# Kernel optimization log

Measured on AMD Instinct MI355X. Metric: run time of the kernel, lower is better.

## Reference

```python
import jax, jax.numpy as jnp
import numpy as np

B, N, D = 4, 4096, 1024
HEADS, DIM_HEAD = 16, 64
INNER = HEADS * DIM_HEAD
LN_EPS = 1e-5


def next_fast_len(n):
    # smallest 5-smooth integer >= n (matches scipy.fftpack.next_fast_len)
    while True:
        m = n
        for p in (2, 3, 5):
            while m % p == 0:
                m //= p
        if m == 1:
            return n
        n += 1


def setup_inputs() -> dict:
    key = jax.random.key(0)
    k = jax.random.split(key, 6)
    x = jax.random.normal(k[0], (B, N, D), dtype=jnp.float32)
    gamma = jnp.ones((D,), dtype=jnp.float32)
    beta = jnp.zeros((D,), dtype=jnp.float32)
    alpha = jax.random.normal(k[1], (HEADS,), dtype=jnp.float32)
    w_in = jax.random.normal(k[2], (INNER, D), dtype=jnp.float32) * 0.02
    w_out = jax.random.normal(k[3], (D, INNER), dtype=jnp.float32) * 0.02
    return {"x": x, "gamma": gamma, "beta": beta, "alpha": alpha, "w_in": w_in, "w_out": w_out}


def reference(x, gamma, beta, alpha, w_in, w_out):
    b, n, d = x.shape
    h, dh = HEADS, DIM_HEAD
    # LayerNorm (biased variance, eps=1e-5)
    mu = jnp.mean(x, axis=-1, keepdims=True)
    var = jnp.var(x, axis=-1, keepdims=True)
    xn = (x - mu) * jax.lax.rsqrt(var + LN_EPS) * gamma + beta
    # project_in (no bias), split heads: b n (h d) -> b h n d
    xi = jnp.einsum('bnd,ed->bne', xn, w_in)
    xi = xi.reshape(b, n, h, dh).transpose(0, 2, 1, 3)  # [b,h,n,dh]
    # exponential decay weights per head: alpha * (1-alpha)**flip(arange(n)) -> [h, n]
    a = jax.nn.sigmoid(alpha)[:, None]
    weights = a * (1.0 - a) ** jnp.arange(n - 1, -1, -1, dtype=x.dtype)[None, :]
    # FFT-based causal correlation (conv1d_fft)
    fast_len = next_fast_len(n + n - 1)
    f_x = jnp.fft.rfft(xi, n=fast_len, axis=-2)           # [b,h,L',dh] complex
    f_w = jnp.fft.rfft(weights, n=fast_len, axis=-1)      # [h,L'] complex
    out = jnp.fft.irfft(f_x * jnp.conj(f_w)[None, :, :, None], fast_len, axis=-2)
    out = jnp.roll(out, -1, axis=-2)
    out = out[:, :, fast_len - n:, :]                      # last n positions -> [b,h,n,dh]
    # merge heads and project out
    out = out.transpose(0, 2, 1, 3).reshape(b, n, h * dh)
    return jnp.einsum('bne,de->bnd', out, w_out)
```

## Files before the change

kernel.cpp:

```cpp
#include <hip/hip_runtime.h>
#include <hip/hip_bf16.h>

#define B_ 4
#define N_ 4096
#define D_ 1024
#define H_ 16
#define INNER_ 1024
#define M_ (B_ * N_)
#define CH_ 128
#define CL_ 32

using bf16x8 = __attribute__((ext_vector_type(8))) __bf16;
using f32x4  = __attribute__((ext_vector_type(4))) float;

__device__ __forceinline__ float bf2f(unsigned short v) {
  return __uint_as_float(((unsigned)v) << 16);
}
__device__ __forceinline__ unsigned short f2bf(float f) {
  __hip_bfloat16 h = __float2bfloat16(f);
  return *reinterpret_cast<unsigned short*>(&h);
}
__device__ __forceinline__ float sigm(float x) { return 1.f / (1.f + expf(-x)); }

__device__ __forceinline__ void gload_lds16(const void* g, void* l) {
  __builtin_amdgcn_global_load_lds(
      (const __attribute__((address_space(1))) unsigned int*)g,
      (__attribute__((address_space(3))) unsigned int*)l, 16, 0, 0);
}

#define W4_ ((INNER_ * D_) / 4)
__global__ __launch_bounds__(256) void cast2_kernel(
    const float* __restrict__ wa, const float* __restrict__ wb,
    __hip_bfloat16* __restrict__ oa, __hip_bfloat16* __restrict__ ob) {
  int i = blockIdx.x * 256 + threadIdx.x;
  const float* src = (i < W4_) ? wa : wb;
  __hip_bfloat16* dst = (i < W4_) ? oa : ob;
  int j = (i < W4_) ? i : i - W4_;
  float4 v = reinterpret_cast<const float4*>(src)[j];
  ushort4 o;
  o.x = f2bf(v.x); o.y = f2bf(v.y); o.z = f2bf(v.z); o.w = f2bf(v.w);
  reinterpret_cast<ushort4*>(dst)[j] = o;
}

__global__ __launch_bounds__(256) void ln_kernel(
    const float* __restrict__ x, const float* __restrict__ gamma,
    const float* __restrict__ beta, __hip_bfloat16* __restrict__ xn) {
  const long row = blockIdx.x;
  const int t = threadIdx.x;
  const float4 v = reinterpret_cast<const float4*>(x + row * D_)[t];
  float s = v.x + v.y + v.z + v.w;
  float s2 = v.x * v.x + v.y * v.y + v.z * v.z + v.w * v.w;
#pragma unroll
  for (int o = 32; o > 0; o >>= 1) {
    s += __shfl_down(s, o);
    s2 += __shfl_down(s2, o);
  }
  __shared__ float red[8];
  const int lane = t & 63, wv = t >> 6;
  if (lane == 0) { red[wv] = s; red[4 + wv] = s2; }
  __syncthreads();
  const float sum = red[0] + red[1] + red[2] + red[3];
  const float sum2 = red[4] + red[5] + red[6] + red[7];
  const float mu = sum * (1.f / D_);
  const float var = sum2 * (1.f / D_) - mu * mu;
  const float rs = rsqrtf(var + 1e-5f);
  const float4 g = reinterpret_cast<const float4*>(gamma)[t];
  const float4 bb = reinterpret_cast<const float4*>(beta)[t];
  ushort4 o;
  o.x = f2bf((v.x - mu) * rs * g.x + bb.x);
  o.y = f2bf((v.y - mu) * rs * g.y + bb.y);
  o.z = f2bf((v.z - mu) * rs * g.z + bb.z);
  o.w = f2bf((v.w - mu) * rs * g.w + bb.w);
  reinterpret_cast<ushort4*>(xn + row * D_)[t] = o;
}

__device__ __forceinline__ void stc(float* p, float v) { *p = v; }
__device__ __forceinline__ void stc(__hip_bfloat16* p, float v) { *p = __float2bfloat16(v); }

template <typename TOUT, int NT>
__global__ __launch_bounds__(512, 2) void gemm256_kernel(
    const __hip_bfloat16* __restrict__ A, const __hip_bfloat16* __restrict__ Bt,
    TOUT* __restrict__ C, int M, int N, int K) {
  static_assert(NT >= 4, "ring needs >=4 tiles");
  __shared__ __align__(16) char lds[131072];
  const int tid = threadIdx.x;
  const int lane = tid & 63;
  const int wave = tid >> 6;

  int wg = blockIdx.y * gridDim.x + blockIdx.x;
  wg = (wg & 7) * 32 + (wg >> 3);
  const int bx = wg & 3;
  const int by = wg >> 2;
  const long bm = (long)by * 256;
  const long bn = (long)bx * 256;

  const int u0  = (tid & 7) ^ ((tid >> 3) & 7);
  const int r0  = 2 * (tid >> 3) + (u0 >> 2);
  const int ck0 = u0 & 3;
  const __hip_bfloat16* sA0 = A  + (bm + r0) * (long)K + ck0 * 8;
  const __hip_bfloat16* sA1 = sA0 + 128l * K;
  const __hip_bfloat16* sB0 = Bt + (bn + r0) * (long)K + ck0 * 8;
  const __hip_bfloat16* sB1 = sB0 + 128l * K;
  char* dbase = (char*)lds + wave * 1024;

  const int wm = wave >> 2;
  const int wn = wave & 3;
  const int fr = lane & 15;
  const int ck = lane >> 4;
  const int pos = (((fr & 1) << 2) | ck) ^ ((fr >> 1) & 7);
  const int laneA = wm * 8192 + (fr >> 1) * 128 + pos * 16;
  const int laneB = 16384 + wn * 4096 + (fr >> 1) * 128 + pos * 16;

  f32x4 acc[8][4] = {};

#define STAGE_A(kt) do { const int _s = (kt) & 3;                         \
    gload_lds16(sA0 + (long)(kt) * 32, dbase + _s * 32768);               \
    gload_lds16(sA1 + (long)(kt) * 32, dbase + _s * 32768 + 8192); } while (0)
#define STAGE_B(kt) do { const int _s = (kt) & 3;                         \
    gload_lds16(sB0 + (long)(kt) * 32, dbase + _s * 32768 + 16384);       \
    gload_lds16(sB1 + (long)(kt) * 32, dbase + _s * 32768 + 24576); } while (0)
#define SBAR() asm volatile("s_barrier" ::: "memory")
#define SCHED0() __builtin_amdgcn_sched_barrier(0)

  STAGE_A(0); STAGE_B(0);
  STAGE_A(1); STAGE_B(1);
  asm volatile("s_waitcnt vmcnt(4)" ::: "memory");
  SBAR();

#pragma unroll 4
  for (int t = 0; t < NT; ++t) {
    const char* base = (const char*)lds + (t & 3) * 32768;
    bf16x8 bv[4], av[4], av2[4];
#pragma unroll
    for (int c = 0; c < 4; ++c) bv[c] = *(const bf16x8*)(base + laneB + c * 1024);
#pragma unroll
    for (int r = 0; r < 4; ++r) av[r] = *(const bf16x8*)(base + laneA + r * 1024);
    if (t + 2 < NT) STAGE_A(t + 2);
    SCHED0();
    SBAR();
    asm volatile("s_waitcnt lgkmcnt(0)" ::: "memory");
    SCHED0();
    __builtin_amdgcn_s_setprio(1);
#pragma unroll
    for (int r = 0; r < 4; ++r)
#pragma unroll
      for (int c = 0; c < 4; ++c)
        acc[r][c] = __builtin_amdgcn_mfma_f32_16x16x32_bf16(av[r], bv[c], acc[r][c], 0, 0, 0);
    __builtin_amdgcn_s_setprio(0);
    SCHED0();
    SBAR();
#pragma unroll
    for (int r = 0; r < 4; ++r) av2[r] = *(const bf16x8*)(base + laneA + (r + 4) * 1024);
    if (t + 2 < NT) STAGE_B(t + 2);
    SCHED0();
    SBAR();
    asm volatile("s_waitcnt lgkmcnt(0)" ::: "memory");
    SCHED0();
    __builtin_amdgcn_s_setprio(1);
#pragma unroll
    for (int r = 0; r < 4; ++r)
#pragma unroll
      for (int c = 0; c < 4; ++c)
        acc[r + 4][c] = __builtin_amdgcn_mfma_f32_16x16x32_bf16(av2[r], bv[c], acc[r + 4][c], 0, 0, 0);
    __builtin_amdgcn_s_setprio(0);
    SCHED0();
    if (t < NT - 2)       asm volatile("s_waitcnt vmcnt(4)" ::: "memory");
    else if (t == NT - 2) asm volatile("s_waitcnt vmcnt(0)" ::: "memory");
    SBAR();
  }
#undef STAGE_A
#undef STAGE_B
#undef SBAR
#undef SCHED0

  const int cr = ck * 4;
#pragma unroll
  for (int rf = 0; rf < 8; ++rf)
#pragma unroll
    for (int cf = 0; cf < 4; ++cf)
#pragma unroll
      for (int r = 0; r < 4; ++r) {
        const long row = bm + wm * 128 + rf * 16 + cr + r;
        const long col = bn + wn * 64 + cf * 16 + fr;
        stc(&C[row * (long)N + col], acc[rf][cf][r]);
      }
}

__global__ __launch_bounds__(256) void scan_finals_kernel(
    const __hip_bfloat16* __restrict__ xi, float* __restrict__ finals,
    const float* __restrict__ alpha) {
  const int e0 = threadIdx.x * 4;
  const int c = blockIdx.y;
  const int b = blockIdx.z;
  const float a = sigm(alpha[e0 >> 6]);
  const float om = 1.f - a;
  long base = ((long)b * N_ + (long)c * CL_) * INNER_ + e0;
  float y0 = 0.f, y1 = 0.f, y2 = 0.f, y3 = 0.f;
  for (int t = 0; t < CL_; ++t) {
    ushort4 u = *(const ushort4*)(xi + base);
    y0 = om * y0 + a * bf2f(u.x);
    y1 = om * y1 + a * bf2f(u.y);
    y2 = om * y2 + a * bf2f(u.z);
    y3 = om * y3 + a * bf2f(u.w);
    base += INNER_;
  }
  float4 f4 = make_float4(y0, y1, y2, y3);
  *reinterpret_cast<float4*>(&finals[((long)b * CH_ + c) * INNER_ + e0]) = f4;
}

__global__ __launch_bounds__(256) void scan_carry_kernel(
    const float* __restrict__ finals, float* __restrict__ carries,
    const float* __restrict__ alpha) {
  const int g = blockIdx.x * 256 + threadIdx.x;
  const int b = g >> 10;
  const int e = g & 1023;
  const float a = sigm(alpha[e >> 6]);
  const float dc = powf(1.f - a, (float)CL_);
  float carry = 0.f;
  for (int c = 0; c < CH_; ++c) {
    const long idx = ((long)b * CH_ + c) * INNER_ + e;
    carries[idx] = carry;
    carry = finals[idx] + dc * carry;
  }
}

__global__ __launch_bounds__(256) void scan_apply_kernel(
    const __hip_bfloat16* __restrict__ xi, __hip_bfloat16* __restrict__ y,
    const float* __restrict__ carries, const float* __restrict__ alpha) {
  const int e0 = threadIdx.x * 4;
  const int c = blockIdx.y;
  const int b = blockIdx.z;
  const float a = sigm(alpha[e0 >> 6]);
  const float om = 1.f - a;
  const float4 cr = *reinterpret_cast<const float4*>(
      &carries[((long)b * CH_ + c) * INNER_ + e0]);
  float y0 = cr.x, y1 = cr.y, y2 = cr.z, y3 = cr.w;
  long base = ((long)b * N_ + (long)c * CL_) * INNER_ + e0;
  for (int t = 0; t < CL_; ++t) {
    ushort4 u = *(const ushort4*)(xi + base);
    y0 = om * y0 + a * bf2f(u.x);
    y1 = om * y1 + a * bf2f(u.y);
    y2 = om * y2 + a * bf2f(u.z);
    y3 = om * y3 + a * bf2f(u.w);
    ushort4 o;
    o.x = f2bf(y0); o.y = f2bf(y1); o.z = f2bf(y2); o.w = f2bf(y3);
    *(ushort4*)(y + base) = o;
    base += INNER_;
  }
}

extern "C" void kernel_launch(void* const* d_in, const int* in_sizes, int n_in,
                              void* d_out, int out_size, void* d_ws, size_t ws_size,
                              hipStream_t stream) {
  const float* x     = (const float*)d_in[0];
  const float* gamma = (const float*)d_in[1];
  const float* beta  = (const float*)d_in[2];
  const float* alpha = (const float*)d_in[3];
  const float* w_in  = (const float*)d_in[4];
  const float* w_out = (const float*)d_in[5];
  float* out = (float*)d_out;
  char* ws = (char*)d_ws;

  __hip_bfloat16* xn = (__hip_bfloat16*)ws;
  __hip_bfloat16* wi = (__hip_bfloat16*)(ws + (32l << 20));
  __hip_bfloat16* wo = (__hip_bfloat16*)(ws + (34l << 20));
  float* finals      = (float*)(ws + (36l << 20));
  float* carries     = (float*)(ws + (38l << 20));
  __hip_bfloat16* xi = (__hip_bfloat16*)d_out;

  cast2_kernel<<<2048, 256, 0, stream>>>(w_in, w_out, wi, wo);

  ln_kernel<<<M_, 256, 0, stream>>>(x, gamma, beta, xn);

  gemm256_kernel<__hip_bfloat16, 32>
      <<<dim3(INNER_ / 256, M_ / 256), 512, 0, stream>>>(xn, wi, xi, M_, INNER_, D_);

  __hip_bfloat16* y = xn;
  scan_finals_kernel<<<dim3(1, CH_, B_), 256, 0, stream>>>(xi, finals, alpha);
  scan_carry_kernel<<<(B_ * INNER_) / 256, 256, 0, stream>>>(finals, carries, alpha);
  scan_apply_kernel<<<dim3(1, CH_, B_), 256, 0, stream>>>(xi, y, carries, alpha);

  gemm256_kernel<float, 32>
      <<<dim3(D_ / 256, M_ / 256), 512, 0, stream>>>(y, wo, out, M_, D_, INNER_);
}
```

Before: 132.9 us.

## Load GEMM B operand directly from global into registers, halve LDS ring

```diff
diff --git a/kernel.cpp b/kernel.cpp
--- a/kernel.cpp
+++ b/kernel.cpp
@@ -78,11 +78,11 @@
 __device__ __forceinline__ void stc(__hip_bfloat16* p, float v) { *p = __float2bfloat16(v); }
 
 template <typename TOUT, int NT>
-__global__ __launch_bounds__(512, 2) void gemm256_kernel(
+__global__ __launch_bounds__(512, 1) void gemm256_kernel(
     const __hip_bfloat16* __restrict__ A, const __hip_bfloat16* __restrict__ Bt,
     TOUT* __restrict__ C, int M, int N, int K) {
-  static_assert(NT >= 4, "ring needs >=4 tiles");
-  __shared__ __align__(16) char lds[131072];
+  static_assert(NT >= 4 && (NT % 4) == 0, "ring needs multiple-of-4 tiles");
+  __shared__ __align__(16) char lds[65536];
   const int tid = threadIdx.x;
   const int lane = tid & 63;
   const int wave = tid >> 6;
@@ -97,10 +97,8 @@
   const int u0  = (tid & 7) ^ ((tid >> 3) & 7);
   const int r0  = 2 * (tid >> 3) + (u0 >> 2);
   const int ck0 = u0 & 3;
-  const __hip_bfloat16* sA0 = A  + (bm + r0) * (long)K + ck0 * 8;
+  const __hip_bfloat16* sA0 = A + (bm + r0) * (long)K + ck0 * 8;
   const __hip_bfloat16* sA1 = sA0 + 128l * K;
-  const __hip_bfloat16* sB0 = Bt + (bn + r0) * (long)K + ck0 * 8;
-  const __hip_bfloat16* sB1 = sB0 + 128l * K;
   char* dbase = (char*)lds + wave * 1024;
 
   const int wm = wave >> 2;
@@ -109,69 +107,64 @@
   const int ck = lane >> 4;
   const int pos = (((fr & 1) << 2) | ck) ^ ((fr >> 1) & 7);
   const int laneA = wm * 8192 + (fr >> 1) * 128 + pos * 16;
-  const int laneB = 16384 + wn * 4096 + (fr >> 1) * 128 + pos * 16;
+  const __hip_bfloat16* gBv = Bt + (bn + wn * 64 + fr) * (long)K + ck * 8;
 
   f32x4 acc[8][4] = {};
 
 #define STAGE_A(kt) do { const int _s = (kt) & 3;                         \
-    gload_lds16(sA0 + (long)(kt) * 32, dbase + _s * 32768);               \
-    gload_lds16(sA1 + (long)(kt) * 32, dbase + _s * 32768 + 8192); } while (0)
-#define STAGE_B(kt) do { const int _s = (kt) & 3;                         \
-    gload_lds16(sB0 + (long)(kt) * 32, dbase + _s * 32768 + 16384);       \
-    gload_lds16(sB1 + (long)(kt) * 32, dbase + _s * 32768 + 24576); } while (0)
+    gload_lds16(sA0 + (long)(kt) * 32, dbase + _s * 16384);               \
+    gload_lds16(sA1 + (long)(kt) * 32, dbase + _s * 16384 + 8192); } while (0)
+#define BVL(dst, kt) do {                                                  \
+    dst[0] = *(const bf16x8*)(gBv + (long)(kt) * 32);                      \
+    dst[1] = *(const bf16x8*)(gBv + (long)(kt) * 32 + 16l * K);            \
+    dst[2] = *(const bf16x8*)(gBv + (long)(kt) * 32 + 32l * K);            \
+    dst[3] = *(const bf16x8*)(gBv + (long)(kt) * 32 + 48l * K); } while (0)
+#define AVL(av, tt) do { const char* _b = (const char*)lds + ((tt) & 3) * 16384; \
+    _Pragma("unroll")                                                      \
+    for (int r = 0; r < 8; ++r) av[r] = *(const bf16x8*)(_b + laneA + r * 1024); } while (0)
+#define MFMA32(av, bv, ro) do {                                            \
+    __builtin_amdgcn_s_setprio(1);                                         \
+    _Pragma("unroll")                                                      \
+    for (int r = 0; r < 8; ++r)                                            \
+      _Pragma("unroll")                                                    \
+      for (int c = 0; c < 4; ++c)                                          \
+        acc[r][c] = __builtin_amdgcn_mfma_f32_16x16x32_bf16(av[r], bv[c], acc[r][c], 0, 0, 0); \
+    __builtin_amdgcn_s_setprio(0); } while (0)
 #define SBAR() asm volatile("s_barrier" ::: "memory")
-#define SCHED0() __builtin_amdgcn_sched_barrier(0)
-
-  STAGE_A(0); STAGE_B(0);
-  STAGE_A(1); STAGE_B(1);
-  asm volatile("s_waitcnt vmcnt(4)" ::: "memory");
+#define WAIT6() asm volatile("s_waitcnt vmcnt(6)" ::: "memory")
+
+  bf16x8 bv0[4], bv1[4];
+  STAGE_A(0); STAGE_A(1);
+  BVL(bv0, 0);
+  WAIT6();
   SBAR();
 
-#pragma unroll 4
-  for (int t = 0; t < NT; ++t) {
-    const char* base = (const char*)lds + (t & 3) * 32768;
-    bf16x8 bv[4], av[4], av2[4];
-#pragma unroll
-    for (int c = 0; c < 4; ++c) bv[c] = *(const bf16x8*)(base + laneB + c * 1024);
-#pragma unroll
-    for (int r = 0; r < 4; ++r) av[r] = *(const bf16x8*)(base + laneA + r * 1024);
-    if (t + 2 < NT) STAGE_A(t + 2);
-    SCHED0();
-    SBAR();
-    asm volatile("s_waitcnt lgkmcnt(0)" ::: "memory");
-    SCHED0();
-    __builtin_amdgcn_s_setprio(1);
-#pragma unroll
-    for (int r = 0; r < 4; ++r)
-#pragma unroll
-      for (int c = 0; c < 4; ++c)
-        acc[r][c] = __builtin_amdgcn_mfma_f32_16x16x32_bf16(av[r], bv[c], acc[r][c], 0, 0, 0);
-    __builtin_amdgcn_s_setprio(0);
-    SCHED0();
-    SBAR();
-#pragma unroll
-    for (int r = 0; r < 4; ++r) av2[r] = *(const bf16x8*)(base + laneA + (r + 4) * 1024);
-    if (t + 2 < NT) STAGE_B(t + 2);
-    SCHED0();
-    SBAR();
-    asm volatile("s_waitcnt lgkmcnt(0)" ::: "memory");
-    SCHED0();
-    __builtin_amdgcn_s_setprio(1);
-#pragma unroll
-    for (int r = 0; r < 4; ++r)
-#pragma unroll
-      for (int c = 0; c < 4; ++c)
-        acc[r + 4][c] = __builtin_amdgcn_mfma_f32_16x16x32_bf16(av2[r], bv[c], acc[r + 4][c], 0, 0, 0);
-    __builtin_amdgcn_s_setprio(0);
-    SCHED0();
-    if (t < NT - 2)       asm volatile("s_waitcnt vmcnt(4)" ::: "memory");
-    else if (t == NT - 2) asm volatile("s_waitcnt vmcnt(0)" ::: "memory");
-    SBAR();
+#pragma unroll 2
+  for (int t = 0; t < NT; t += 2) {
+    {
+      bf16x8 av[8];
+      AVL(av, t);
+      if (t + 2 < NT) STAGE_A(t + 2);
+      BVL(bv1, t + 1);
+      MFMA32(av, bv0, 0);
+      WAIT6();
+      SBAR();
+    }
+    {
+      bf16x8 av[8];
+      AVL(av, t + 1);
+      if (t + 3 < NT) STAGE_A(t + 3);
+      if (t + 2 < NT) BVL(bv0, t + 2);
+      MFMA32(av, bv1, 0);
+      if (t + 2 < NT) { WAIT6(); SBAR(); }
+    }
   }
 #undef STAGE_A
-#undef STAGE_B
+#undef BVL
+#undef AVL
+#undef MFMA32
 #undef SBAR
-#undef SCHED0
+#undef WAIT6
 
   const int cr = ck * 4;
 #pragma unroll
```

Measured after the change: 171.0 us. 28.7% more time.

## Restructure GEMM into 64-deep K tiles with quadrant-split 8-wave ping-pong pipeline

Applied to the files above, without the earlier changes.

```diff
diff --git a/kernel.cpp b/kernel.cpp
--- a/kernel.cpp
+++ b/kernel.cpp
@@ -78,10 +78,9 @@
 __device__ __forceinline__ void stc(__hip_bfloat16* p, float v) { *p = __float2bfloat16(v); }
 
 template <typename TOUT, int NT>
-__global__ __launch_bounds__(512, 2) void gemm256_kernel(
+__global__ __launch_bounds__(512, 2) void gemm256p8_kernel(
     const __hip_bfloat16* __restrict__ A, const __hip_bfloat16* __restrict__ Bt,
     TOUT* __restrict__ C, int M, int N, int K) {
-  static_assert(NT >= 4, "ring needs >=4 tiles");
   __shared__ __align__(16) char lds[131072];
   const int tid = threadIdx.x;
   const int lane = tid & 63;
@@ -94,96 +93,110 @@
   const long bm = (long)by * 256;
   const long bn = (long)bx * 256;
 
-  const int u0  = (tid & 7) ^ ((tid >> 3) & 7);
-  const int r0  = 2 * (tid >> 3) + (u0 >> 2);
-  const int ck0 = u0 & 3;
-  const __hip_bfloat16* sA0 = A  + (bm + r0) * (long)K + ck0 * 8;
-  const __hip_bfloat16* sA1 = sA0 + 128l * K;
-  const __hip_bfloat16* sB0 = Bt + (bn + r0) * (long)K + ck0 * 8;
-  const __hip_bfloat16* sB1 = sB0 + 128l * K;
-  char* dbase = (char*)lds + wave * 1024;
-
-  const int wm = wave >> 2;
-  const int wn = wave & 3;
-  const int fr = lane & 15;
-  const int ck = lane >> 4;
-  const int pos = (((fr & 1) << 2) | ck) ^ ((fr >> 1) & 7);
-  const int laneA = wm * 8192 + (fr >> 1) * 128 + pos * 16;
-  const int laneB = 16384 + wn * 4096 + (fr >> 1) * 128 + pos * 16;
+  const int ckl = ((tid & 7) ^ ((tid >> 3) & 7)) * 8;
+  const __hip_bfloat16* sA = A  + (bm + (tid >> 3)) * (long)K + ckl;
+  const __hip_bfloat16* sB = Bt + (bn + (tid >> 3)) * (long)K + ckl;
+  char* dA = (char*)lds + wave * 1024;
+  char* dB = (char*)lds + 65536 + wave * 1024;
+
+  const int wm = wave >> 2, wn = wave & 3;
+  const int fr = lane & 15, q = lane >> 4;
+  const int pp0 = (q ^ (fr & 7)) << 4;
+  const int pp1 = ((q ^ (fr & 7)) ^ 4) << 4;
+  const char* ldsc = (const char*)lds;
+  const int rowA = (wm * 64 + fr) * 128;
+  const int rowB = 65536 + (wn * 32 + fr) * 128;
 
   f32x4 acc[8][4] = {};
 
-#define STAGE_A(kt) do { const int _s = (kt) & 3;                         \
-    gload_lds16(sA0 + (long)(kt) * 32, dbase + _s * 32768);               \
-    gload_lds16(sA1 + (long)(kt) * 32, dbase + _s * 32768 + 8192); } while (0)
-#define STAGE_B(kt) do { const int _s = (kt) & 3;                         \
-    gload_lds16(sB0 + (long)(kt) * 32, dbase + _s * 32768 + 16384);       \
-    gload_lds16(sB1 + (long)(kt) * 32, dbase + _s * 32768 + 24576); } while (0)
-#define SBAR() asm volatile("s_barrier" ::: "memory")
-#define SCHED0() __builtin_amdgcn_sched_barrier(0)
-
-  STAGE_A(0); STAGE_B(0);
-  STAGE_A(1); STAGE_B(1);
+#define STG_A(h) do {                                                        \
+    const long _o = (long)(((h) & 1) * 128) * K + ((h) >> 1) * 64;           \
+    char* _d = dA + ((h) & 3) * 16384;                                       \
+    gload_lds16(sA + _o, _d);                                                \
+    gload_lds16(sA + _o + 64l * K, _d + 8192); } while (0)
+#define STG_B(h) do {                                                        \
+    const long _o = (long)(((h) & 1) * 128) * K + ((h) >> 1) * 64;           \
+    char* _d = dB + ((h) & 3) * 16384;                                       \
+    gload_lds16(sB + _o, _d);                                                \
+    gload_lds16(sB + _o + 64l * K, _d + 8192); } while (0)
+#define RD_A(av, sl) do { _Pragma("unroll")                                  \
+    for (int f = 0; f < 4; ++f) {                                            \
+      av[f * 2 + 0] = *(const bf16x8*)(ldsc + (sl) * 16384 + rowA + f * 2048 + pp0); \
+      av[f * 2 + 1] = *(const bf16x8*)(ldsc + (sl) * 16384 + rowA + f * 2048 + pp1); } } while (0)
+#define RD_B(bv, sl) do { _Pragma("unroll")                                  \
+    for (int g = 0; g < 2; ++g) {                                            \
+      bv[g * 2 + 0] = *(const bf16x8*)(ldsc + (sl) * 16384 + rowB + g * 2048 + pp0); \
+      bv[g * 2 + 1] = *(const bf16x8*)(ldsc + (sl) * 16384 + rowB + g * 2048 + pp1); } } while (0)
+#define MFMA_Q(rq, cq, av, bv) do {                                          \
+    __builtin_amdgcn_s_setprio(1);                                           \
+    _Pragma("unroll")                                                        \
+    for (int kb = 0; kb < 2; ++kb)                                           \
+      _Pragma("unroll")                                                      \
+      for (int f = 0; f < 4; ++f)                                            \
+        _Pragma("unroll")                                                    \
+        for (int g = 0; g < 2; ++g)                                          \
+          acc[(rq) * 4 + f][(cq) * 2 + g] = __builtin_amdgcn_mfma_f32_16x16x32_bf16( \
+              av[f * 2 + kb], bv[g * 2 + kb], acc[(rq) * 4 + f][(cq) * 2 + g], 0, 0, 0); \
+    __builtin_amdgcn_s_setprio(0); } while (0)
+#define SBAR()  asm volatile("s_barrier" ::: "memory")
+#define LGKM0() do { asm volatile("s_waitcnt lgkmcnt(0)" ::: "memory");      \
+    __builtin_amdgcn_sched_barrier(0); } while (0)
+
+  STG_A(0); STG_B(0); STG_A(1); STG_B(1);
+  STG_A(2); STG_B(2);
   asm volatile("s_waitcnt vmcnt(4)" ::: "memory");
   SBAR();
 
-#pragma unroll 4
+#pragma unroll 2
   for (int t = 0; t < NT; ++t) {
-    const char* base = (const char*)lds + (t & 3) * 32768;
-    bf16x8 bv[4], av[4], av2[4];
-#pragma unroll
-    for (int c = 0; c < 4; ++c) bv[c] = *(const bf16x8*)(base + laneB + c * 1024);
-#pragma unroll
-    for (int r = 0; r < 4; ++r) av[r] = *(const bf16x8*)(base + laneA + r * 1024);
-    if (t + 2 < NT) STAGE_A(t + 2);
-    SCHED0();
-    SBAR();
-    asm volatile("s_waitcnt lgkmcnt(0)" ::: "memory");
-    SCHED0();
-    __builtin_amdgcn_s_setprio(1);
-#pragma unroll
-    for (int r = 0; r < 4; ++r)
-#pragma unroll
-      for (int c = 0; c < 4; ++c)
-        acc[r][c] = __builtin_amdgcn_mfma_f32_16x16x32_bf16(av[r], bv[c], acc[r][c], 0, 0, 0);
-    __builtin_amdgcn_s_setprio(0);
-    SCHED0();
-    SBAR();
-#pragma unroll
-    for (int r = 0; r < 4; ++r) av2[r] = *(const bf16x8*)(base + laneA + (r + 4) * 1024);
-    if (t + 2 < NT) STAGE_B(t + 2);
-    SCHED0();
-    SBAR();
-    asm volatile("s_waitcnt lgkmcnt(0)" ::: "memory");
-    SCHED0();
-    __builtin_amdgcn_s_setprio(1);
-#pragma unroll
-    for (int r = 0; r < 4; ++r)
-#pragma unroll
-      for (int c = 0; c < 4; ++c)
-        acc[r + 4][c] = __builtin_amdgcn_mfma_f32_16x16x32_bf16(av2[r], bv[c], acc[r + 4][c], 0, 0, 0);
-    __builtin_amdgcn_s_setprio(0);
-    SCHED0();
-    if (t < NT - 2)       asm volatile("s_waitcnt vmcnt(4)" ::: "memory");
-    else if (t == NT - 2) asm volatile("s_waitcnt vmcnt(0)" ::: "memory");
-    SBAR();
-  }
-#undef STAGE_A
-#undef STAGE_B
+    const int s0 = (2 * t) & 3, s1 = (2 * t + 1) & 3;
+    bf16x8 av[8], bv0[4], bv1[4];
+    RD_A(av, s0); RD_B(bv0, s0);
+    if (t < NT - 1) { STG_A(2 * t + 3); STG_B(2 * t + 3); }
+    asm volatile("s_waitcnt lgkmcnt(8)" ::: "memory");
+    SBAR();
+    LGKM0();
+    MFMA_Q(0, 0, av, bv0);
+    SBAR();
+    RD_B(bv1, s1);
+    SBAR();
+    LGKM0();
+    MFMA_Q(0, 1, av, bv1);
+    SBAR();
+    RD_A(av, s1);
+    if (t < NT - 2) STG_A(2 * t + 4);
+    SBAR();
+    LGKM0();
+    MFMA_Q(1, 0, av, bv0);
+    SBAR();
+    if (t < NT - 2) STG_B(2 * t + 4);
+    SBAR();
+    MFMA_Q(1, 1, av, bv1);
+    asm volatile("s_waitcnt vmcnt(4)" ::: "memory");
+    SBAR();
+  }
+#undef STG_A
+#undef STG_B
+#undef RD_A
+#undef RD_B
+#undef MFMA_Q
 #undef SBAR
-#undef SCHED0
-
-  const int cr = ck * 4;
-#pragma unroll
-  for (int rf = 0; rf < 8; ++rf)
-#pragma unroll
-    for (int cf = 0; cf < 4; ++cf)
-#pragma unroll
-      for (int r = 0; r < 4; ++r) {
-        const long row = bm + wm * 128 + rf * 16 + cr + r;
-        const long col = bn + wn * 64 + cf * 16 + fr;
-        stc(&C[row * (long)N + col], acc[rf][cf][r]);
-      }
+#undef LGKM0
+
+#pragma unroll
+  for (int rq = 0; rq < 2; ++rq)
+#pragma unroll
+    for (int f = 0; f < 4; ++f)
+#pragma unroll
+      for (int cq = 0; cq < 2; ++cq)
+#pragma unroll
+        for (int g = 0; g < 2; ++g)
+#pragma unroll
+          for (int r = 0; r < 4; ++r) {
+            const long row = bm + rq * 128 + wm * 64 + f * 16 + q * 4 + r;
+            const long col = bn + cq * 128 + wn * 32 + g * 16 + fr;
+            stc(&C[row * (long)N + col], acc[rq * 4 + f][cq * 2 + g][r]);
+          }
 }
 
 __global__ __launch_bounds__(256) void scan_finals_kernel(
@@ -272,7 +285,7 @@
 
   ln_kernel<<<M_, 256, 0, stream>>>(x, gamma, beta, xn);
 
-  gemm256_kernel<__hip_bfloat16, 32>
+  gemm256p8_kernel<__hip_bfloat16, 16>
       <<<dim3(INNER_ / 256, M_ / 256), 512, 0, stream>>>(xn, wi, xi, M_, INNER_, D_);
 
   __hip_bfloat16* y = xn;
@@ -280,6 +293,6 @@
   scan_carry_kernel<<<(B_ * INNER_) / 256, 256, 0, stream>>>(finals, carries, alpha);
   scan_apply_kernel<<<dim3(1, CH_, B_), 256, 0, stream>>>(xi, y, carries, alpha);
 
-  gemm256_kernel<float, 32>
+  gemm256p8_kernel<float, 16>
       <<<dim3(D_ / 256, M_ / 256), 512, 0, stream>>>(y, wo, out, M_, D_, INNER_);
 }
```

Result: faster. 130.1 us (-2.1%).
